# Kernel tuning notes

Measured on AMD Instinct MI355X. Metric: run time of the kernel, lower is better.

## Reference

```python
import jax, jax.numpy as jnp
import numpy as np

DIM = 5120
NUM_HEADS = 40
HEAD_DIM = DIM // NUM_HEADS
EPS = 1e-6


def rms_norm(x, g):
    # RMSNorm over last dim in fp32 for stability
    xf = x.astype(jnp.float32)
    inv = jax.lax.rsqrt(jnp.mean(xf * xf, axis=-1, keepdims=True) + EPS)
    return (xf * inv).astype(x.dtype) * g


def setup_inputs() -> dict:
    key = jax.random.key(0)
    ks = jax.random.split(key, 12)
    B, S, L = 1, 4096, 512
    inp = {
        "hidden_cond": jax.random.normal(ks[0], (B, S, DIM), jnp.float32),
        "hidden_uncond": jax.random.normal(ks[1], (B, S, DIM), jnp.float32),
        "context_cond": jax.random.normal(ks[2], (B, L, DIM), jnp.float32),
        "context_uncond": jax.random.normal(ks[3], (B, L, DIM), jnp.float32),
        # parameters (torch nn.Linear: y = x @ W.T + b)
        "Wq": jax.random.normal(ks[4], (DIM, DIM), jnp.float32) * (DIM ** -0.5),
        "bq": jnp.zeros((DIM,), jnp.float32),
        "Wkv": jax.random.normal(ks[5], (2 * DIM, DIM), jnp.float32) * (DIM ** -0.5),
        "bkv": jnp.zeros((2 * DIM,), jnp.float32),
        "gq": jnp.ones((DIM,), jnp.float32),
        "gk": jnp.ones((DIM,), jnp.float32),
        "Wo": jax.random.normal(ks[6], (DIM, DIM), jnp.float32) * (DIM ** -0.5),
        "bo": jnp.zeros((DIM,), jnp.float32),
    }
    return inp


def reference(hidden_cond, hidden_uncond, context_cond, context_uncond,
              Wq, bq, Wkv, bkv, gq, gk, Wo, bo):
    H, Dh = NUM_HEADS, HEAD_DIM
    scale = Dh ** -0.5

    hidden = jnp.concatenate([hidden_cond, hidden_uncond], axis=0)   # [2B, S, D]
    context = jnp.concatenate([context_cond, context_uncond], axis=0)  # [2B, L, D]
    CB, S, D = hidden.shape
    L = context.shape[1]

    q = hidden @ Wq.T + bq                    # [2B, S, D]
    q = rms_norm(q, gq)
    q = q.reshape(CB, S, H, Dh).transpose(0, 2, 1, 3)  # [2B, H, S, Dh]

    kv = context @ Wkv.T + bkv                # [2B, L, 2D]
    kv = kv.reshape(CB, L, 2, H, Dh).transpose(2, 0, 3, 1, 4)  # [2,2B,H,L,Dh]
    k, v = kv[0], kv[1]

    k_flat = k.transpose(0, 2, 1, 3).reshape(CB, L, D)
    k_flat = rms_norm(k_flat, gk)
    k = k_flat.reshape(CB, L, H, Dh).transpose(0, 2, 1, 3)  # [2B, H, L, Dh]

    attn = jnp.einsum('bhsd,bhld->bhsl', q, k) * scale
    attn = jax.nn.softmax(attn.astype(jnp.float32), axis=-1).astype(q.dtype)
    out = jnp.einsum('bhsl,bhld->bhsd', attn, v)            # [2B, H, S, Dh]
    out = out.transpose(0, 2, 1, 3).reshape(CB, S, D)
    out = out @ Wo.T + bo

    out_cond, out_uncond = jnp.split(out, 2, axis=0)
    return (out_cond, out_uncond)
```

## Files before the change

kernel.cpp:

```cpp
#include <hip/hip_runtime.h>
#include <hip/hip_bf16.h>
#include <cstdint>
#include <cstddef>

#define DIM 5120
#define NH 40
#define HD 128
#define S_LEN 4096
#define L_LEN 512
#define CBATCH 2
#define MQ (CBATCH*S_LEN)
#define ML (CBATCH*L_LEN)

typedef unsigned short ushort_t;
typedef __bf16 bf16x8 __attribute__((ext_vector_type(8)));
typedef float f32x4 __attribute__((ext_vector_type(4)));
typedef float f32x16 __attribute__((ext_vector_type(16)));

__device__ __forceinline__ ushort_t f2bf(float f) {
  union { float f; unsigned u; } c; c.f = f;
  unsigned r = c.u + 0x7fffu + ((c.u >> 16) & 1u);
  return (ushort_t)(r >> 16);
}

__device__ __forceinline__ void load_lds16(const void* g, void* l) {
  __builtin_amdgcn_global_load_lds(
      (const __attribute__((address_space(1))) void*)g,
      (__attribute__((address_space(3))) void*)l, 16, 0, 0);
}

__global__ __launch_bounds__(256) void cvt_f32_bf16(const float* __restrict__ in,
                                                    ushort_t* __restrict__ out, int n4) {
  int i = blockIdx.x * 256 + threadIdx.x;
  if (i >= n4) return;
  float4 v = *(const float4*)(in + 4ull * (size_t)i);
  ushort4 o;
  o.x = f2bf(v.x); o.y = f2bf(v.y); o.z = f2bf(v.z); o.w = f2bf(v.w);
  *(ushort4*)(out + 4ull * (size_t)i) = o;
}

template <int OUT_F32>
__global__ __launch_bounds__(512, 2) void gemm_bt8(const ushort_t* __restrict__ A,
                                                   const ushort_t* __restrict__ W,
                                                   const float* __restrict__ bias,
                                                   void* __restrict__ Cout,
                                                   int M, int N, int K) {
  __shared__ ushort_t lds[73728];
  char* ldsc = (char*)lds;
  const int tid = threadIdx.x;
  const int lane = tid & 63, w = tid >> 6;
  const int g = lane >> 4, c = lane & 15;
  const int wm = w >> 2, wn = w & 3;
  const int ntn = N >> 8;
  const int nwg = gridDim.x;
  int bid = blockIdx.x;
  bid = (bid & 7) * (nwg >> 3) + (bid >> 3);
  const int tm = bid / ntn, tn = bid % ntn;
  const size_t m0 = (size_t)tm * 256, n0 = (size_t)tn * 256;
  const ushort_t* Ab = A + m0 * (size_t)K;
  const ushort_t* Bb = W + n0 * (size_t)K;
  const int NT = K >> 6;

  const int srow = tid >> 2;
  const int sgq  = (tid & 3) ^ (((tid >> 5) & 1) << 1);
  const size_t rb0 = (size_t)srow * K + (size_t)sgq * 8;
  const size_t rb1 = rb0 + (size_t)128 * K;
  const int d0 = tid * 16;

  int offA[8], offB[4];
#pragma unroll
  for (int m = 0; m < 8; ++m) {
    int row = wm * 128 + m * 16 + c;
    offA[m] = row * 64 + ((g * 16) ^ ((row & 8) << 2));
  }
#pragma unroll
  for (int n = 0; n < 4; ++n) {
    int row = wn * 64 + n * 16 + c;
    offB[n] = row * 64 + ((g * 16) ^ ((row & 8) << 2));
  }

  auto STAGE = [&](int tIdx, int j, int dOff) {
    const size_t kof = (size_t)tIdx * 64 + (size_t)((j >> 1) << 5);
    const ushort_t* gsrc = ((j & 1) ? Ab : Bb) + kof;
    char* db = ldsc + dOff;
    load_lds16(gsrc + rb0, db + d0);
    load_lds16(gsrc + rb1, db + 8192 + d0);
  };
  auto nx = [](int x) { return (x + 16384 == 147456) ? 0 : x + 16384; };

  f32x4 acc[8][4] = {};

#pragma unroll
  for (int h = 0; h < 8; ++h) STAGE(h >> 2, h & 3, h * 16384);
  asm volatile("s_waitcnt vmcnt(8)" ::: "memory");
  __builtin_amdgcn_s_barrier();

  int rd = 0;
  int sOff = 131072;
  for (int t = 0; t < NT; ++t) {
    const int r0 = rd, r1 = nx(r0), r2 = nx(r1), r3 = nx(r2);
    bf16x8 a[4], a2[4], b[4];
#pragma unroll
    for (int m = 0; m < 4; ++m) a[m] = *(const bf16x8*)(ldsc + r1 + offA[m]);
#pragma unroll
    for (int n = 0; n < 4; ++n) b[n] = *(const bf16x8*)(ldsc + r0 + offB[n]);
    if (t < NT - 2) { STAGE(t + 2, 0, sOff); sOff = nx(sOff); }
    __builtin_amdgcn_s_barrier();
    asm volatile("s_waitcnt lgkmcnt(0)" ::: "memory");
    __builtin_amdgcn_sched_barrier(0);
    __builtin_amdgcn_s_setprio(1);
#pragma unroll
    for (int m = 0; m < 4; ++m)
#pragma unroll
      for (int n = 0; n < 4; ++n)
        acc[m][n] = __builtin_amdgcn_mfma_f32_16x16x32_bf16(a[m], b[n], acc[m][n], 0, 0, 0);
    __builtin_amdgcn_s_setprio(0);
    __builtin_amdgcn_s_barrier();
#pragma unroll
    for (int m = 0; m < 4; ++m) a2[m] = *(const bf16x8*)(ldsc + r1 + offA[4 + m]);
    if (t < NT - 2) { STAGE(t + 2, 1, sOff); sOff = nx(sOff); }
    __builtin_amdgcn_s_barrier();
    asm volatile("s_waitcnt lgkmcnt(0)" ::: "memory");
    __builtin_amdgcn_sched_barrier(0);
    __builtin_amdgcn_s_setprio(1);
#pragma unroll
    for (int m = 0; m < 4; ++m)
#pragma unroll
      for (int n = 0; n < 4; ++n)
        acc[4 + m][n] = __builtin_amdgcn_mfma_f32_16x16x32_bf16(a2[m], b[n], acc[4 + m][n], 0, 0, 0);
    __builtin_amdgcn_s_setprio(0);
    __builtin_amdgcn_s_barrier();
#pragma unroll
    for (int m = 0; m < 4; ++m) a[m] = *(const bf16x8*)(ldsc + r3 + offA[m]);
#pragma unroll
    for (int n = 0; n < 4; ++n) b[n] = *(const bf16x8*)(ldsc + r2 + offB[n]);
    if (t < NT - 2) { STAGE(t + 2, 2, sOff); sOff = nx(sOff); }
    __builtin_amdgcn_s_barrier();
    asm volatile("s_waitcnt lgkmcnt(0)" ::: "memory");
    __builtin_amdgcn_sched_barrier(0);
    __builtin_amdgcn_s_setprio(1);
#pragma unroll
    for (int m = 0; m < 4; ++m)
#pragma unroll
      for (int n = 0; n < 4; ++n)
        acc[m][n] = __builtin_amdgcn_mfma_f32_16x16x32_bf16(a[m], b[n], acc[m][n], 0, 0, 0);
    __builtin_amdgcn_s_setprio(0);
    __builtin_amdgcn_s_barrier();
#pragma unroll
    for (int m = 0; m < 4; ++m) a2[m] = *(const bf16x8*)(ldsc + r3 + offA[4 + m]);
    if (t < NT - 2) { STAGE(t + 2, 3, sOff); sOff = nx(sOff); }
    __builtin_amdgcn_s_barrier();
    asm volatile("s_waitcnt lgkmcnt(0)" ::: "memory");
    __builtin_amdgcn_sched_barrier(0);
    __builtin_amdgcn_s_setprio(1);
#pragma unroll
    for (int m = 0; m < 4; ++m)
#pragma unroll
      for (int n = 0; n < 4; ++n)
        acc[4 + m][n] = __builtin_amdgcn_mfma_f32_16x16x32_bf16(a2[m], b[n], acc[4 + m][n], 0, 0, 0);
    __builtin_amdgcn_s_setprio(0);
    if (t < NT - 2)       asm volatile("s_waitcnt vmcnt(6)" ::: "memory");
    else if (t == NT - 2) asm volatile("s_waitcnt vmcnt(0)" ::: "memory");
    __builtin_amdgcn_s_barrier();
    rd = nx(r3);
  }

#pragma unroll
  for (int m = 0; m < 8; ++m) {
#pragma unroll
    for (int n = 0; n < 4; ++n) {
      size_t gm = m0 + wm * 128 + m * 16 + g * 4;
      size_t gn = n0 + wn * 64 + n * 16 + c;
      float bn = bias[gn];
#pragma unroll
      for (int r = 0; r < 4; ++r) {
        float v = acc[m][n][r] + bn;
        if (OUT_F32) ((float*)Cout)[(gm + r) * (size_t)N + gn] = v;
        else         ((ushort_t*)Cout)[(gm + r) * (size_t)N + gn] = f2bf(v);
      }
    }
  }
  (void)M;
}

template <int OUT_F32>
__global__ __launch_bounds__(256) void gemm_bt(const ushort_t* __restrict__ A,
                                               const ushort_t* __restrict__ W,
                                               const float* __restrict__ bias,
                                               void* __restrict__ Cout,
                                               int M, int N, int K) {
  __shared__ ushort_t sA[128 * 32];
  __shared__ ushort_t sB[128 * 32];
  const int tid = threadIdx.x;
  const int w = tid >> 6, lane = tid & 63;
  const int g = lane >> 4, c = lane & 15;
  const int ntn = N >> 7;
  const int nwg = gridDim.x;
  int bid = blockIdx.x;
  bid = (bid & 7) * (nwg >> 3) + (bid >> 3);
  const int tm = bid / ntn, tn = bid % ntn;
  const size_t m0 = (size_t)tm * 128, n0 = (size_t)tn * 128;
  const int wr = (w >> 1) * 64, wc = (w & 1) * 64;

  f32x4 acc[4][4] = {};

  const ushort_t* Abase = A + m0 * (size_t)K;
  const ushort_t* Bbase = W + n0 * (size_t)K;

  for (int k0 = 0; k0 < K; k0 += 32) {
    __syncthreads();
#pragma unroll
    for (int i = 0; i < 2; ++i) {
      int gid = i * 256 + tid;
      int row = gid >> 2, colE = (gid & 3) << 3;
      load_lds16(Abase + (size_t)row * K + k0 + colE, sA + i * 2048 + w * 512);
      load_lds16(Bbase + (size_t)row * K + k0 + colE, sB + i * 2048 + w * 512);
    }
    __syncthreads();
    bf16x8 a[4], b[4];
#pragma unroll
    for (int m = 0; m < 4; ++m)
      a[m] = *(const bf16x8*)(sA + (wr + m * 16 + c) * 32 + g * 8);
#pragma unroll
    for (int n = 0; n < 4; ++n)
      b[n] = *(const bf16x8*)(sB + (wc + n * 16 + c) * 32 + g * 8);
#pragma unroll
    for (int m = 0; m < 4; ++m)
#pragma unroll
      for (int n = 0; n < 4; ++n)
        acc[m][n] = __builtin_amdgcn_mfma_f32_16x16x32_bf16(a[m], b[n], acc[m][n], 0, 0, 0);
  }

#pragma unroll
  for (int m = 0; m < 4; ++m) {
#pragma unroll
    for (int n = 0; n < 4; ++n) {
      size_t gm = m0 + wr + m * 16 + g * 4;
      size_t gn = n0 + wc + n * 16 + c;
      float bn = bias[gn];
#pragma unroll
      for (int r = 0; r < 4; ++r) {
        float v = acc[m][n][r] + bn;
        if (OUT_F32) ((float*)Cout)[(gm + r) * (size_t)N + gn] = v;
        else         ((ushort_t*)Cout)[(gm + r) * (size_t)N + gn] = f2bf(v);
      }
    }
  }
}

__global__ __launch_bounds__(256) void rmsnorm_rows(ushort_t* __restrict__ x,
                                                    const float* __restrict__ gw,
                                                    int ncols, int stride, float oscale) {
  const int row = blockIdx.x;
  ushort_t* p = x + (size_t)row * stride;
  const int tid = threadIdx.x;
  const int nch = ncols >> 3;
  float ss = 0.f;
  for (int ci = tid; ci < nch; ci += 256) {
    bf16x8 v = *(const bf16x8*)(p + ci * 8);
#pragma unroll
    for (int j = 0; j < 8; ++j) { float f = (float)v[j]; ss += f * f; }
  }
#pragma unroll
  for (int off = 1; off < 64; off <<= 1) ss += __shfl_xor(ss, off);
  __shared__ float sred[4];
  if ((tid & 63) == 0) sred[tid >> 6] = ss;
  __syncthreads();
  float tot = sred[0] + sred[1] + sred[2] + sred[3];
  float inv = rsqrtf(tot / (float)ncols + 1e-6f) * oscale;
  for (int ci = tid; ci < nch; ci += 256) {
    bf16x8 v = *(const bf16x8*)(p + ci * 8);
    bf16x8 ov;
#pragma unroll
    for (int j = 0; j < 8; ++j) {
      float f = (float)v[j];
      ushort_t ob = f2bf(f * inv * gw[ci * 8 + j]);
      ov[j] = *(__bf16*)&ob;
    }
    *(bf16x8*)(p + ci * 8) = ov;
  }
}

__global__ __launch_bounds__(256) void transpose_v(const ushort_t* __restrict__ kv,
                                                   ushort_t* __restrict__ vt) {
  const int bh = blockIdx.y, b = bh / NH, h = bh % NH;
  const int l0 = blockIdx.x * 32;
  const ushort_t* src = kv + (size_t)b * L_LEN * (2 * DIM) + DIM + (size_t)h * HD;
  ushort_t* dst = vt + (size_t)bh * HD * L_LEN;
  __shared__ ushort_t tile[32][HD + 16];
  const int tid = threadIdx.x;
#pragma unroll
  for (int i = 0; i < 2; ++i) {
    int gid = i * 256 + tid;
    int r = gid >> 4, ce = (gid & 15) << 3;
    *(bf16x8*)(&tile[r][ce]) = *(const bf16x8*)(src + (size_t)(l0 + r) * (2 * DIM) + ce);
  }
  __syncthreads();
#pragma unroll
  for (int i = 0; i < 2; ++i) {
    int gid = i * 256 + tid;
    int d = gid >> 2, le = (gid & 3) << 3;
    bf16x8 v;
#pragma unroll
    for (int j = 0; j < 8; ++j) v[j] = *(__bf16*)&tile[le + j][d];
    *(bf16x8*)(dst + (size_t)d * L_LEN + l0 + le) = v;
  }
}

__global__ __launch_bounds__(256) void attn_fwd(const ushort_t* __restrict__ q,
                                                const ushort_t* __restrict__ kv,
                                                const ushort_t* __restrict__ vt,
                                                ushort_t* __restrict__ out) {
  const int bh = blockIdx.y, b = bh / NH, h = bh % NH;
  const int tid = threadIdx.x, w = tid >> 6, lane = tid & 63;
  const int lq = lane & 31, hi = lane >> 5;
  const int qr0 = blockIdx.x * 128 + w * 32;

  const ushort_t* qrow  = q  + ((size_t)b * S_LEN + qr0 + lq) * DIM + (size_t)h * HD + hi * 8;
  const ushort_t* krow  = kv + (size_t)b * L_LEN * (2 * DIM) + (size_t)h * HD
                             + (size_t)lq * (2 * DIM) + hi * 8;
  const ushort_t* vrow  = vt + (size_t)bh * HD * L_LEN + (size_t)lq * L_LEN + hi * 8;

  bf16x8 qf[8];
#pragma unroll
  for (int ks = 0; ks < 8; ++ks) qf[ks] = *(const bf16x8*)(qrow + ks * 16);

  f32x16 o[4];
#pragma unroll
  for (int ch = 0; ch < 4; ++ch) o[ch] = 0.f;
  float m = -1e30f, lsum = 0.f;

  for (int l0 = 0; l0 < L_LEN; l0 += 32) {
    f32x16 sv = 0.f;
#pragma unroll
    for (int ks = 0; ks < 8; ++ks) {
      bf16x8 kf = *(const bf16x8*)(krow + (size_t)l0 * (2 * DIM) + ks * 16);
      sv = __builtin_amdgcn_mfma_f32_32x32x16_bf16(kf, qf[ks], sv, 0, 0, 0);
    }
    float pm = fmaxf(fmaxf(fmaxf(sv[0], sv[1]), fmaxf(sv[2], sv[3])),
                     fmaxf(fmaxf(sv[4], sv[5]), fmaxf(sv[6], sv[7])));
    pm = fmaxf(pm, fmaxf(fmaxf(fmaxf(sv[8], sv[9]), fmaxf(sv[10], sv[11])),
                         fmaxf(fmaxf(sv[12], sv[13]), fmaxf(sv[14], sv[15]))));
    pm = fmaxf(pm, __shfl_xor(pm, 32));
    if (__ballot(pm > m + 8.0f)) {
      float mn = fmaxf(m, pm);
      float al = __builtin_amdgcn_exp2f(m - mn);
      lsum *= al;
      m = mn;
#pragma unroll
      for (int r = 0; r < 16; ++r) {
        float ar = __shfl(al, (r & 3) + 8 * (r >> 2) + 4 * hi);
        o[0][r] *= ar; o[1][r] *= ar; o[2][r] *= ar; o[3][r] *= ar;
      }
    }
    float p[16]; float ls = 0.f;
#pragma unroll
    for (int r = 0; r < 16; ++r) { p[r] = __builtin_amdgcn_exp2f(sv[r] - m); ls += p[r]; }
    ls += __shfl_xor(ls, 32);
    lsum += ls;
    bf16x8 pa[2];
#pragma unroll
    for (int ks = 0; ks < 2; ++ks) {
      unsigned w0 = (unsigned)f2bf(p[8 * ks + 0]) | ((unsigned)f2bf(p[8 * ks + 1]) << 16);
      unsigned w1 = (unsigned)f2bf(p[8 * ks + 2]) | ((unsigned)f2bf(p[8 * ks + 3]) << 16);
      unsigned w2 = (unsigned)f2bf(p[8 * ks + 4]) | ((unsigned)f2bf(p[8 * ks + 5]) << 16);
      unsigned w3 = (unsigned)f2bf(p[8 * ks + 6]) | ((unsigned)f2bf(p[8 * ks + 7]) << 16);
      unsigned e0 = __shfl_xor((int)w0, 32), e1 = __shfl_xor((int)w1, 32);
      unsigned e2 = __shfl_xor((int)w2, 32), e3 = __shfl_xor((int)w3, 32);
      unsigned d0 = hi ? e2 : w0, d1 = hi ? e3 : w1;
      unsigned d2 = hi ? w2 : e0, d3 = hi ? w3 : e1;
      unsigned tmp[4] = {d0, d1, d2, d3};
      pa[ks] = *(const bf16x8*)tmp;
    }
#pragma unroll
    for (int ch = 0; ch < 4; ++ch) {
#pragma unroll
      for (int ks = 0; ks < 2; ++ks) {
        bf16x8 vf = *(const bf16x8*)(vrow + (size_t)ch * 32 * L_LEN + l0 + ks * 16);
        o[ch] = __builtin_amdgcn_mfma_f32_32x32x16_bf16(pa[ks], vf, o[ch], 0, 0, 0);
      }
    }
  }

  float inv[16];
#pragma unroll
  for (int r = 0; r < 16; ++r) {
    float lr = __shfl(lsum, (r & 3) + 8 * (r >> 2) + 4 * hi);
    inv[r] = 1.0f / lr;
  }
  ushort_t* ob = out + ((size_t)b * S_LEN + qr0) * DIM + (size_t)h * HD;
#pragma unroll
  for (int ch = 0; ch < 4; ++ch)
#pragma unroll
    for (int r = 0; r < 16; ++r) {
      int row = (r & 3) + 8 * (r >> 2) + 4 * hi;
      ob[(size_t)row * DIM + ch * 32 + lq] = f2bf(o[ch][r] * inv[r]);
    }
}

extern "C" void kernel_launch(void* const* d_in, const int* in_sizes, int n_in,
                              void* d_out, int out_size, void* d_ws, size_t ws_size,
                              hipStream_t stream) {
  (void)in_sizes; (void)n_in; (void)out_size; (void)ws_size;
  const float* hidden_c = (const float*)d_in[0];
  const float* hidden_u = (const float*)d_in[1];
  const float* ctx_c    = (const float*)d_in[2];
  const float* ctx_u    = (const float*)d_in[3];
  const float* Wq  = (const float*)d_in[4];
  const float* bq  = (const float*)d_in[5];
  const float* Wkv = (const float*)d_in[6];
  const float* bkv = (const float*)d_in[7];
  const float* gq  = (const float*)d_in[8];
  const float* gk  = (const float*)d_in[9];
  const float* Wo  = (const float*)d_in[10];
  const float* bo  = (const float*)d_in[11];

  char* ws = (char*)d_ws;
  size_t off = 0;
  auto alloc = [&](size_t bytes) {
    char* p = ws + off; off += (bytes + 255) & ~(size_t)255; return p;
  };
  ushort_t* hbf  = (ushort_t*)alloc((size_t)MQ * DIM * 2);
  ushort_t* cbf  = (ushort_t*)alloc((size_t)ML * DIM * 2);
  ushort_t* wqb  = (ushort_t*)alloc((size_t)DIM * DIM * 2);
  ushort_t* wkvb = (ushort_t*)alloc((size_t)2 * DIM * DIM * 2);
  ushort_t* kvb  = (ushort_t*)alloc((size_t)ML * 2 * DIM * 2);
  ushort_t* vtb  = (ushort_t*)alloc((size_t)CBATCH * NH * HD * L_LEN * 2);
  ushort_t* qb   = (ushort_t*)d_out;

  auto cvt = [&](const float* in, ushort_t* o, size_t n) {
    int n4 = (int)(n >> 2);
    cvt_f32_bf16<<<dim3((n4 + 255) / 256), dim3(256), 0, stream>>>(in, o, n4);
  };
  cvt(hidden_c, hbf, (size_t)S_LEN * DIM);
  cvt(hidden_u, hbf + (size_t)S_LEN * DIM, (size_t)S_LEN * DIM);
  cvt(ctx_c, cbf, (size_t)L_LEN * DIM);
  cvt(ctx_u, cbf + (size_t)L_LEN * DIM, (size_t)L_LEN * DIM);
  cvt(Wq, wqb, (size_t)DIM * DIM);
  cvt(Wkv, wkvb, (size_t)2 * DIM * DIM);

  gemm_bt8<0><<<dim3((MQ / 256) * (DIM / 256)), dim3(512), 0, stream>>>(
      hbf, wqb, bq, (void*)qb, MQ, DIM, DIM);
  gemm_bt<0><<<dim3((ML / 128) * ((2 * DIM) / 128)), dim3(256), 0, stream>>>(
      cbf, wkvb, bkv, (void*)kvb, ML, 2 * DIM, DIM);
  cvt(Wo, wqb, (size_t)DIM * DIM);

  const float qscale = 0.08838834764831845f * 1.4426950408889634f;
  rmsnorm_rows<<<dim3(MQ), dim3(256), 0, stream>>>(qb, gq, DIM, DIM, qscale);
  rmsnorm_rows<<<dim3(ML), dim3(256), 0, stream>>>(kvb, gk, DIM, 2 * DIM, 1.0f);
  transpose_v<<<dim3(L_LEN / 32, CBATCH * NH), dim3(256), 0, stream>>>(kvb, vtb);

  attn_fwd<<<dim3(S_LEN / 128, CBATCH * NH), dim3(256), 0, stream>>>(qb, kvb, vtb, hbf);

  gemm_bt8<1><<<dim3((MQ / 256) * (DIM / 256)), dim3(512), 0, stream>>>(
      hbf, wqb, bo, d_out, MQ, DIM, DIM);
}
```

Measured before the change: 1.598 ms.

## Stage K/V tiles through double-buffered shared memory in attention kernel

The attention kernel's four waves each loaded K and V fragments directly from global memory. It now cooperatively loads each 32-row K/V tile into LDS once per block, using a layout that matches the MFMA fragment reads. The next tile is prefetched into registers while the current one is computed, then written to the alternate buffer. This cuts redundant global traffic across waves and hides load latency, at the cost of 32 KB of LDS and a barrier per tile.

```diff
diff --git a/kernel.cpp b/kernel.cpp
--- a/kernel.cpp
+++ b/kernel.cpp
@@ -316,11 +316,20 @@
   const int lq = lane & 31, hi = lane >> 5;
   const int qr0 = blockIdx.x * 128 + w * 32;
 
-  const ushort_t* qrow  = q  + ((size_t)b * S_LEN + qr0 + lq) * DIM + (size_t)h * HD + hi * 8;
-  const ushort_t* krow  = kv + (size_t)b * L_LEN * (2 * DIM) + (size_t)h * HD
-                             + (size_t)lq * (2 * DIM) + hi * 8;
-  const ushort_t* vrow  = vt + (size_t)bh * HD * L_LEN + (size_t)lq * L_LEN + hi * 8;
-
+  __shared__ ushort_t sK[2][4096];
+  __shared__ ushort_t sV[2][4096];
+
+  const int skl = tid >> 3, skc = tid & 7;
+  const ushort_t* kgsrc = kv + ((size_t)b * L_LEN + skl) * (2 * DIM)
+                             + (size_t)h * HD + skc * 16;
+  ushort_t* kd0 = &sK[0][(skc * 2) * 256 + skl * 8];
+  ushort_t* kd1 = &sK[0][(skc * 2 + 1) * 256 + skl * 8];
+  const int svd = tid >> 1, svh = tid & 1;
+  const ushort_t* vgsrc = vt + (size_t)bh * HD * L_LEN + (size_t)svd * L_LEN + svh * 16;
+  ushort_t* vd0 = &sV[0][(svh * 2) * 1024 + svd * 8];
+  ushort_t* vd1 = &sV[0][(svh * 2 + 1) * 1024 + svd * 8];
+
+  const ushort_t* qrow = q + ((size_t)b * S_LEN + qr0 + lq) * DIM + (size_t)h * HD + hi * 8;
   bf16x8 qf[8];
 #pragma unroll
   for (int ks = 0; ks < 8; ++ks) qf[ks] = *(const bf16x8*)(qrow + ks * 16);
@@ -330,11 +339,34 @@
   for (int ch = 0; ch < 4; ++ch) o[ch] = 0.f;
   float m = -1e30f, lsum = 0.f;
 
-  for (int l0 = 0; l0 < L_LEN; l0 += 32) {
+  {
+    uint4 ka = *(const uint4*)kgsrc;
+    uint4 kb = *(const uint4*)(kgsrc + 8);
+    uint4 va = *(const uint4*)vgsrc;
+    uint4 vb = *(const uint4*)(vgsrc + 8);
+    *(uint4*)kd0 = ka; *(uint4*)kd1 = kb;
+    *(uint4*)vd0 = va; *(uint4*)vd1 = vb;
+  }
+  __syncthreads();
+
+  const int NT = L_LEN / 32;
+  int buf = 0;
+  for (int t = 0; t < NT; ++t) {
+    uint4 ka, kb, va, vb;
+    if (t + 1 < NT) {
+      const ushort_t* kg = kgsrc + (size_t)(t + 1) * 32 * (2 * DIM);
+      const ushort_t* vg = vgsrc + (t + 1) * 32;
+      ka = *(const uint4*)kg; kb = *(const uint4*)(kg + 8);
+      va = *(const uint4*)vg; vb = *(const uint4*)(vg + 8);
+    }
+
+    const ushort_t* kbuf = sK[buf];
+    const ushort_t* vbuf = sV[buf];
+
     f32x16 sv = 0.f;
 #pragma unroll
     for (int ks = 0; ks < 8; ++ks) {
-      bf16x8 kf = *(const bf16x8*)(krow + (size_t)l0 * (2 * DIM) + ks * 16);
+      bf16x8 kf = *(const bf16x8*)(kbuf + (ks * 2 + hi) * 256 + lq * 8);
       sv = __builtin_amdgcn_mfma_f32_32x32x16_bf16(kf, qf[ks], sv, 0, 0, 0);
     }
     float pm = fmaxf(fmaxf(fmaxf(sv[0], sv[1]), fmaxf(sv[2], sv[3])),
@@ -376,10 +408,18 @@
     for (int ch = 0; ch < 4; ++ch) {
 #pragma unroll
       for (int ks = 0; ks < 2; ++ks) {
-        bf16x8 vf = *(const bf16x8*)(vrow + (size_t)ch * 32 * L_LEN + l0 + ks * 16);
+        bf16x8 vf = *(const bf16x8*)(vbuf + (ks * 2 + hi) * 1024 + (ch * 32 + lq) * 8);
         o[ch] = __builtin_amdgcn_mfma_f32_32x32x16_bf16(pa[ks], vf, o[ch], 0, 0, 0);
       }
     }
+
+    if (t + 1 < NT) {
+      const int nb = buf ^ 1;
+      *(uint4*)(kd0 + nb * 4096) = ka; *(uint4*)(kd1 + nb * 4096) = kb;
+      *(uint4*)(vd0 + nb * 4096) = va; *(uint4*)(vd1 + nb * 4096) = vb;
+    }
+    __syncthreads();
+    buf ^= 1;
   }
 
   float inv[16];
```

Measured after the change: 1.432 ms. 1.12x faster.
